# Optimization experiments

Measured on AMD Instinct MI355X. Metric: run time of the kernel, lower is better.

Reference implementation:

```python
import jax, jax.numpy as jnp
import numpy as np

B, LQ, S, D, H = 8, 1024, 256, 1024, 16
HD = D // H
LN_EPS = 1e-5


def layer_norm(x, g, b):
    m = jnp.mean(x, axis=-1, keepdims=True)
    v = jnp.mean((x - m) ** 2, axis=-1, keepdims=True)
    return (x - m) / jnp.sqrt(v + LN_EPS) * g + b


def setup_inputs() -> dict:
    key = jax.random.key(0)
    ks = jax.random.split(key, 12)
    sc = 0.02
    p = lambda k, shp: jax.random.normal(k, shp, dtype=jnp.float32) * sc
    return {
        "memory": jax.random.normal(ks[0], (B, LQ, D // 2), dtype=jnp.float32),
        "gaze_features": jax.random.normal(ks[1], (B, LQ, D // 2), dtype=jnp.float32),
        "text_features": jax.random.normal(ks[2], (B, S, D), dtype=jnp.float32),
        "w_in": p(ks[3], (3 * D, D)),  # packed q,k,v in_proj (torch MHA layout)
        "b_in": jnp.zeros((3 * D,), jnp.float32),
        "w_o": p(ks[4], (D, D)),
        "b_o": jnp.zeros((D,), jnp.float32),
        "w1": p(ks[5], (D, D)),
        "b1": jnp.zeros((D,), jnp.float32),
        "w2": p(ks[6], (D, D)),
        "b2": jnp.zeros((D,), jnp.float32),
        "g1": jnp.ones((D,), jnp.float32),
        "be1": jnp.zeros((D,), jnp.float32),
        "g2": jnp.ones((D,), jnp.float32),
        "be2": jnp.zeros((D,), jnp.float32),
    }


def reference(memory, gaze_features, text_features, w_in, b_in, w_o, b_o,
              w1, b1, w2, b2, g1, be1, g2, be2):
    combined = jnp.concatenate([memory, gaze_features], axis=-1)  # [B, LQ, D]
    wq, wk, wv = w_in[:D], w_in[D:2 * D], w_in[2 * D:]
    bq, bk, bv = b_in[:D], b_in[D:2 * D], b_in[2 * D:]

    q = (combined @ wq.T + bq).reshape(B, LQ, H, HD)
    k = (text_features @ wk.T + bk).reshape(B, S, H, HD)
    v = (text_features @ wv.T + bv).reshape(B, S, H, HD)

    scores = jnp.einsum("bqhd,bkhd->bhqk", q, k) / jnp.sqrt(jnp.float32(HD))
    attn_w = jax.nn.softmax(scores, axis=-1)
    ctx = jnp.einsum("bhqk,bkhd->bqhd", attn_w, v).reshape(B, LQ, D)
    attn_output = ctx @ w_o.T + b_o  # [B, LQ, D]

    # dual FFN branches share linear1/linear2 (as in the source); dropout = eval identity
    ffn = jax.nn.relu(attn_output @ w1.T + b1) @ w2.T + b2
    refpoint_embed = layer_norm(ffn, g1, be1)
    tgt = layer_norm(ffn, g2, be2)

    # vectorized box decode (replaces the per-element Python loop)
    s = jax.nn.sigmoid(attn_output[..., :4])
    xc, yc, w, h = s[..., 0], s[..., 1], s[..., 2], s[..., 3]
    init_box_proposal = jnp.stack(
        [xc - w / 2, yc - h / 2, xc + w / 2, yc + h / 2], axis=-1)  # [B, LQ, 4]

    return refpoint_embed, tgt, init_box_proposal
```

## Files before the change

### kernel.cpp

```cpp
#include <hip/hip_runtime.h>


typedef unsigned short u16;
typedef unsigned int u32;
typedef __bf16 bf16x8 __attribute__((ext_vector_type(8)));
typedef float f32x4 __attribute__((ext_vector_type(4)));
typedef u16 u16x4 __attribute__((ext_vector_type(4)));

struct CvtArgs { const void* in[15]; };

__device__ __forceinline__ u16 f2bf(float f) {
  u32 u = __builtin_bit_cast(u32, f);
  u += 0x7fffu + ((u >> 16) & 1u);
  return (u16)(u >> 16);
}
__device__ __forceinline__ float bf2f(u16 h) {
  u32 u = ((u32)h) << 16;
  return __builtin_bit_cast(float, u);
}

struct WsPtrs {
  u16 *c_mem, *c_gaze, *c_text, *c_win, *c_bin, *c_wo, *c_bo, *c_w1, *c_b1,
      *c_w2, *c_b2, *c_g1, *c_be1, *c_g2, *c_be2;
  u16 *q, *k, *v, *ctx, *woT, *wf, *bfb, *h1, *ffnb;
};
__device__ __forceinline__ WsPtrs wsp(u16* C) {
  WsPtrs w;
  w.c_mem = C;                 w.c_gaze = C + 4194304;   w.c_text = C + 8388608;
  w.c_win = C + 10485760;      w.c_bin = C + 13631488;   w.c_wo = C + 13634560;
  w.c_bo = C + 14683136;       w.c_w1 = C + 14684160;    w.c_b1 = C + 15732736;
  w.c_w2 = C + 15733760;       w.c_b2 = C + 16782336;    w.c_g1 = C + 16783360;
  w.c_be1 = C + 16784384;      w.c_g2 = C + 16785408;    w.c_be2 = C + 16786432;
  u16* B2 = C + 16787488;
  w.q = B2;                    w.k = B2 + 8388608;       w.v = B2 + 10485760;
  w.ctx = B2 + 12582912;
  w.woT = B2 + 20971520;
  w.wf  = B2 + 22020096;
  w.bfb = B2 + 23068672;
  w.h1  = B2 + 29360128;
  w.ffnb = B2;
  return w;
}

__device__ __forceinline__ void cvt_chunk(bool f32in, u16* dst,
                                          const void* const* srcs, u32 c8) {
  const u32 cum[16] = {0u, 4194304u, 8388608u, 10485760u, 13631488u, 13634560u,
                       14683136u, 14684160u, 15732736u, 15733760u, 16782336u,
                       16783360u, 16784384u, 16785408u, 16786432u, 16787456u};
  u32 base = c8 * 8u;
  int idx = 0;
#pragma unroll
  for (int i = 1; i < 15; ++i) if (base >= cum[i]) idx = i;
  u32 off = base - cum[idx];
  if (f32in) {
    const float* s = (const float*)srcs[idx] + off;
    float4 a = ((const float4*)s)[0];
    float4 b = ((const float4*)s)[1];
    u16 t[8] = {f2bf(a.x), f2bf(a.y), f2bf(a.z), f2bf(a.w),
                f2bf(b.x), f2bf(b.y), f2bf(b.z), f2bf(b.w)};
    *(uint4*)(dst + base) = *(const uint4*)t;
  } else {
    *(uint4*)(dst + base) = *(const uint4*)((const u16*)srcs[idx] + off);
  }
}

__global__ __launch_bounds__(256) void cvt_tr(CvtArgs a, u16* ws) {
  __shared__ u16 tile[128 * 136];
  const bool f32in = (((const u32*)a.in[11])[0] == 0x3F800000u);
  const int bid = blockIdx.x, tid = threadIdx.x;
  if (bid < 64) {
    WsPtrs w = wsp(ws);
    int tr = bid >> 3, tc = bid & 7;
#pragma unroll
    for (int p = 0; p < 8; ++p) {
      int t = p * 16 + (tid >> 4);
      int j8 = (tid & 15) * 8;
      u16 tmp[8];
      if (f32in) {
        const float* s = (const float*)a.in[5] + (size_t)(tr * 128 + t) * 1024 + tc * 128 + j8;
        float4 x = ((const float4*)s)[0], y = ((const float4*)s)[1];
        tmp[0]=f2bf(x.x); tmp[1]=f2bf(x.y); tmp[2]=f2bf(x.z); tmp[3]=f2bf(x.w);
        tmp[4]=f2bf(y.x); tmp[5]=f2bf(y.y); tmp[6]=f2bf(y.z); tmp[7]=f2bf(y.w);
      } else {
        *(uint4*)tmp = *(const uint4*)((const u16*)a.in[5] + (size_t)(tr * 128 + t) * 1024 + tc * 128 + j8);
      }
      *(uint4*)&tile[t * 136 + j8] = *(const uint4*)tmp;
    }
    __syncthreads();
#pragma unroll
    for (int p = 0; p < 8; ++p) {
      int j = p * 16 + (tid >> 4);
      int t8 = (tid & 15) * 8;
      u16 tmp[8];
#pragma unroll
      for (int i = 0; i < 8; ++i) tmp[i] = tile[(t8 + i) * 136 + j];
      *(uint4*)(w.woT + (size_t)(tc * 128 + j) * 1024 + tr * 128 + t8) = *(const uint4*)tmp;
    }
  } else {
    u32 c8 = (u32)(bid - 64) * 256u + tid;
    if (c8 < 2098432u) cvt_chunk(f32in, ws, a.in, c8);
  }
}

__device__ __forceinline__ void gemm_core(
    u16* sA, u16* sB,
    const u16* A0, const u16* A1, int Ksplit, int lda0, int lda1,
    const u16* W, const u16* bias, void* out, int N, int K,
    int mode, int lg, int m0, int n0)
{
  const int tid = threadIdx.x;
  const int wave = tid >> 6, lane = tid & 63;
  const int quad = lane >> 4, l16 = lane & 15;
  const int wm = wave >> 1, wn = wave & 1;

  f32x4 acc[4][4];
#pragma unroll
  for (int i = 0; i < 4; ++i)
#pragma unroll
    for (int j = 0; j < 4; ++j) acc[i][j] = (f32x4){0.f, 0.f, 0.f, 0.f};

  for (int k0 = 0; k0 < K; k0 += 128) {
#pragma unroll
    for (int qi = 0; qi < 8; ++qi) {
      int p = (wave * 8 + qi) * 64 + lane;
      int row = p >> 4;
      int c = (p & 15) ^ (row & 7);
      int gk = k0 + (c << 3);
      const u16* srcA = (gk < Ksplit) ? (A0 + (size_t)(m0 + row) * lda0 + gk)
                                      : (A1 + (size_t)(m0 + row) * lda1 + (gk - Ksplit));
      __builtin_amdgcn_global_load_lds(
          (const __attribute__((address_space(1))) void*)srcA,
          (__attribute__((address_space(3))) void*)&sA[(size_t)(wave * 8 + qi) * 512],
          16, 0, 0);
      const u16* srcB = W + (size_t)(n0 + row) * K + gk;
      __builtin_amdgcn_global_load_lds(
          (const __attribute__((address_space(1))) void*)srcB,
          (__attribute__((address_space(3))) void*)&sB[(size_t)(wave * 8 + qi) * 512],
          16, 0, 0);
    }
    __syncthreads();
#pragma unroll
    for (int ks = 0; ks < 4; ++ks) {
      const int ch = (ks << 2) + quad;
      bf16x8 af[4], bw[4];
#pragma unroll
      for (int i = 0; i < 4; ++i) {
        int row = wm * 64 + i * 16 + l16;
        af[i] = *(const bf16x8*)&sA[(row << 7) + ((ch ^ (row & 7)) << 3)];
      }
#pragma unroll
      for (int j = 0; j < 4; ++j) {
        int row = wn * 64 + j * 16 + l16;
        bw[j] = *(const bf16x8*)&sB[(row << 7) + ((ch ^ (row & 7)) << 3)];
      }
#pragma unroll
      for (int i = 0; i < 4; ++i)
#pragma unroll
        for (int j = 0; j < 4; ++j)
          acc[i][j] = __builtin_amdgcn_mfma_f32_16x16x32_bf16(af[i], bw[j], acc[i][j], 0, 0, 0);
    }
    __syncthreads();
  }

#pragma unroll
  for (int i = 0; i < 4; ++i) {
#pragma unroll
    for (int j = 0; j < 4; ++j) {
      int n = n0 + wn * 64 + j * 16 + l16;
      float bv = bias ? bf2f(bias[n]) : 0.f;
#pragma unroll
      for (int rr = 0; rr < 4; ++rr) {
        int m = m0 + wm * 64 + i * 16 + quad * 4 + rr;
        float val = acc[i][j][rr] + bv;
        if (mode == 1) val = fmaxf(val, 0.f);
        if (mode <= 1) {
          ((u16*)out)[(size_t)m * N + n] = f2bf(val);
        } else if (mode == 3) {
          int b = m >> lg, l = m & ((1 << lg) - 1);
          int h = n >> 6, d = n & 63;
          ((u16*)out)[((size_t)((b * 16 + h)) << (lg + 6)) + (l << 6) + d] = f2bf(val);
        } else {
          int b = m >> lg, s = m & ((1 << lg) - 1);
          int h = n >> 6, d = n & 63;
          ((u16*)out)[((size_t)(((b * 16 + h) << 6) + d) << lg) + s] = f2bf(val);
        }
      }
    }
  }
}

__global__ __launch_bounds__(256) void qkvwf(u16* ws) {
  __shared__ u16 lds[32768];
  WsPtrs w = wsp(ws);
  const int bid = blockIdx.x, tid = threadIdx.x;
  if (bid < 512) {
    gemm_core(lds, lds + 16384, w.c_mem, w.c_gaze, 512, 512, 512,
              w.c_win, w.c_bin, w.q, 1024, 1024, 3, 10,
              (bid >> 3) * 128, (bid & 7) * 128);
  } else if (bid < 640) {
    int u = bid - 512;
    gemm_core(lds, lds + 16384, w.c_text, w.c_text, 1024, 1024, 1024,
              w.c_win + 1048576, w.c_bin + 1024, w.k, 1024, 1024, 3, 8,
              (u >> 3) * 128, (u & 7) * 128);
  } else if (bid < 768) {
    int u = bid - 640;
    gemm_core(lds, lds + 16384, w.c_text, w.c_text, 1024, 1024, 1024,
              w.c_win + 2097152, w.c_bin + 2048, w.v, 1024, 1024, 4, 8,
              (u >> 3) * 128, (u & 7) * 128);
  } else if (bid < 832) {
    int u = bid - 768;
    gemm_core(lds, lds + 16384, w.c_w1, w.c_w1, 1024, 1024, 1024,
              w.woT, nullptr, w.wf, 1024, 1024, 0, 0,
              (u >> 3) * 128, (u & 7) * 128);
  } else {
    int i = (bid - 832) * 256 + tid;
    const u16* w1row = w.c_w1 + (size_t)i * 1024;
    float acc = bf2f(w.c_b1[i]);
    for (int kk = 0; kk < 1024; kk += 8) {
      bf16x8 wv = *(const bf16x8*)(w1row + kk);
      bf16x8 bv = *(const bf16x8*)(w.c_bo + kk);
#pragma unroll
      for (int j = 0; j < 8; ++j) acc += (float)wv[j] * (float)bv[j];
    }
    w.bfb[i] = f2bf(acc);
  }
}

__global__ __launch_bounds__(256) void attn_kernel(u16* ws) {
  __shared__ u16 sV[64 * 256];
  __shared__ u16 sKP[256 * 64];
  WsPtrs w = wsp(ws);
  const int tid = threadIdx.x;
  const int wave = tid >> 6, lane = tid & 63;
  const int quad = lane >> 4, l16 = lane & 15;
  const int qb = blockIdx.x & 15, bh = blockIdx.x >> 4;

  {
    int rr = tid >> 3, c8 = (tid & 7) << 3;
    const u16* kb = w.k + (size_t)bh * 16384;
#pragma unroll
    for (int p = 0; p < 8; ++p) {
      int row = p * 32 + rr;
      uint4 val = *(const uint4*)(kb + row * 64 + c8);
      *(uint4*)&sKP[(row << 6) + ((((c8 >> 3) ^ (row & 7))) << 3)] = val;
    }
    int r2 = tid >> 5, c8b = (tid & 31) << 3;
    const u16* vb = w.v + (size_t)bh * 16384;
#pragma unroll
    for (int p = 0; p < 8; ++p) {
      int row = p * 8 + r2;
      uint4 val = *(const uint4*)(vb + (row << 8) + c8b);
      *(uint4*)&sV[(row << 8) + ((((c8b >> 3) ^ (row & 7))) << 3)] = val;
    }
  }
  bf16x8 aq[2];
  {
    const u16* qrow = w.q + ((size_t)bh * 1024 + qb * 64 + wave * 16 + l16) * 64 + quad * 8;
    aq[0] = *(const bf16x8*)(qrow);
    aq[1] = *(const bf16x8*)(qrow + 32);
  }
  __syncthreads();

  f32x4 sc[16];
#pragma unroll
  for (int nt = 0; nt < 16; ++nt) sc[nt] = (f32x4){0.f, 0.f, 0.f, 0.f};
#pragma unroll
  for (int ks = 0; ks < 2; ++ks) {
    const int ch = (ks << 2) + quad;
#pragma unroll
    for (int nt = 0; nt < 16; ++nt) {
      int row = nt * 16 + l16;
      bf16x8 bk = *(const bf16x8*)&sKP[(row << 6) + ((ch ^ (row & 7)) << 3)];
      sc[nt] = __builtin_amdgcn_mfma_f32_16x16x32_bf16(aq[ks], bk, sc[nt], 0, 0, 0);
    }
  }
#pragma unroll
  for (int rr = 0; rr < 4; ++rr) {
    float mx = -1e30f;
#pragma unroll
    for (int nt = 0; nt < 16; ++nt) mx = fmaxf(mx, sc[nt][rr]);
    for (int off = 1; off < 16; off <<= 1) mx = fmaxf(mx, __shfl_xor(mx, off, 64));
    float sum = 0.f;
#pragma unroll
    for (int nt = 0; nt < 16; ++nt) {
      float p = __expf((sc[nt][rr] - mx) * 0.125f);
      sc[nt][rr] = p; sum += p;
    }
    for (int off = 1; off < 16; off <<= 1) sum += __shfl_xor(sum, off, 64);
    float inv = 1.f / sum;
#pragma unroll
    for (int nt = 0; nt < 16; ++nt) sc[nt][rr] *= inv;
  }
  __syncthreads();
#pragma unroll
  for (int nt = 0; nt < 16; ++nt)
#pragma unroll
    for (int rr = 0; rr < 4; ++rr) {
      int row = wave * 16 + quad * 4 + rr;
      int col = nt * 16 + l16;
      sKP[(row << 8) + (((col >> 3) ^ (row & 7)) << 3) + (col & 7)] = f2bf(sc[nt][rr]);
    }
  __syncthreads();

  f32x4 o[4];
#pragma unroll
  for (int j = 0; j < 4; ++j) o[j] = (f32x4){0.f, 0.f, 0.f, 0.f};
#pragma unroll
  for (int ks = 0; ks < 8; ++ks) {
    const int ch = (ks << 2) + quad;
    int prow = wave * 16 + l16;
    bf16x8 ap = *(const bf16x8*)&sKP[(prow << 8) + ((ch ^ (prow & 7)) << 3)];
#pragma unroll
    for (int j = 0; j < 4; ++j) {
      int vrow = j * 16 + l16;
      bf16x8 bv = *(const bf16x8*)&sV[(vrow << 8) + ((ch ^ (vrow & 7)) << 3)];
      o[j] = __builtin_amdgcn_mfma_f32_16x16x32_bf16(ap, bv, o[j], 0, 0, 0);
    }
  }
  const int b = bh >> 4, h = bh & 15;
#pragma unroll
  for (int j = 0; j < 4; ++j)
#pragma unroll
    for (int rr = 0; rr < 4; ++rr) {
      int m = qb * 64 + wave * 16 + quad * 4 + rr;
      int d = h * 64 + j * 16 + l16;
      w.ctx[((size_t)b * 1024 + m) * 1024 + d] = f2bf(o[j][rr]);
    }
}

__global__ __launch_bounds__(256) void h1box(u16* ws, void* out, const void* g1orig) {
  __shared__ u16 lds[32768];
  WsPtrs w = wsp(ws);
  const int u = blockIdx.x, tid = threadIdx.x;
  const int r16 = tid >> 4, l4 = tid & 15;
  {
    const bool f32out = (((const u32*)g1orig)[0] == 0x3F800000u);
    int m = u * 16 + r16;
    int k0 = l4 * 64;
    const u16* crow = w.ctx + (size_t)m * 1024 + k0;
    float a0 = 0.f, a1 = 0.f, a2 = 0.f, a3 = 0.f;
#pragma unroll
    for (int kk = 0; kk < 64; kk += 8) {
      bf16x8 cv = *(const bf16x8*)(crow + kk);
      bf16x8 w0 = *(const bf16x8*)(w.c_wo + k0 + kk);
      bf16x8 w1 = *(const bf16x8*)(w.c_wo + 1024 + k0 + kk);
      bf16x8 w2 = *(const bf16x8*)(w.c_wo + 2048 + k0 + kk);
      bf16x8 w3 = *(const bf16x8*)(w.c_wo + 3072 + k0 + kk);
#pragma unroll
      for (int j = 0; j < 8; ++j) {
        float c = (float)cv[j];
        a0 += c * (float)w0[j]; a1 += c * (float)w1[j];
        a2 += c * (float)w2[j]; a3 += c * (float)w3[j];
      }
    }
    for (int off = 1; off < 16; off <<= 1) {
      a0 += __shfl_xor(a0, off, 64); a1 += __shfl_xor(a1, off, 64);
      a2 += __shfl_xor(a2, off, 64); a3 += __shfl_xor(a3, off, 64);
    }
    if (l4 == 0) {
      a0 += bf2f(w.c_bo[0]); a1 += bf2f(w.c_bo[1]);
      a2 += bf2f(w.c_bo[2]); a3 += bf2f(w.c_bo[3]);
      float s0 = 1.f / (1.f + __expf(-a0)), s1 = 1.f / (1.f + __expf(-a1));
      float s2 = 1.f / (1.f + __expf(-a2)), s3 = 1.f / (1.f + __expf(-a3));
      float o0 = s0 - s2 * 0.5f, o1 = s1 - s3 * 0.5f;
      float o2 = s0 + s2 * 0.5f, o3 = s1 + s3 * 0.5f;
      if (f32out) {
        float* fo = (float*)out + 16777216;
        *(float4*)(fo + (size_t)m * 4) = make_float4(o0, o1, o2, o3);
      } else {
        u16* bo = (u16*)out + 16777216;
        u16x4 o; o[0] = f2bf(o0); o[1] = f2bf(o1); o[2] = f2bf(o2); o[3] = f2bf(o3);
        *(u16x4*)(bo + (size_t)m * 4) = o;
      }
    }
  }
  gemm_core(lds, lds + 16384, w.ctx, w.ctx, 1024, 1024, 1024,
            w.wf, w.bfb, w.h1, 1024, 1024, 1, 0, (u >> 3) * 128, (u & 7) * 128);
}

__global__ __launch_bounds__(256) void w2gemm(u16* ws) {
  __shared__ u16 lds[32768];
  WsPtrs w = wsp(ws);
  gemm_core(lds, lds + 16384, w.h1, w.h1, 1024, 1024, 1024,
            w.c_w2, w.c_b2, w.ffnb, 1024, 1024, 0, 0,
            (blockIdx.x >> 3) * 128, (blockIdx.x & 7) * 128);
}

__global__ __launch_bounds__(256) void ln_kernel(u16* ws, void* outv, const void* g1orig) {
  WsPtrs w = wsp(ws);
  const bool f32out = (((const u32*)g1orig)[0] == 0x3F800000u);
  const int row = blockIdx.x, tid = threadIdx.x;
  int c = tid * 4;
  u16x4 xr = *(const u16x4*)(w.ffnb + (size_t)row * 1024 + c);
  float x[4] = {bf2f(xr[0]), bf2f(xr[1]), bf2f(xr[2]), bf2f(xr[3])};
  float s = x[0] + x[1] + x[2] + x[3];
  float s2 = x[0]*x[0] + x[1]*x[1] + x[2]*x[2] + x[3]*x[3];
  for (int m = 32; m >= 1; m >>= 1) { s += __shfl_xor(s, m, 64); s2 += __shfl_xor(s2, m, 64); }
  __shared__ float red[8];
  int wv = tid >> 6;
  if ((tid & 63) == 0) { red[wv] = s; red[4 + wv] = s2; }
  __syncthreads();
  s = red[0] + red[1] + red[2] + red[3];
  s2 = red[4] + red[5] + red[6] + red[7];
  float mean = s * (1.f / 1024.f);
  float var = s2 * (1.f / 1024.f) - mean * mean;
  float inv = rsqrtf(var + 1e-5f);
  float y[4] = {(x[0] - mean) * inv, (x[1] - mean) * inv, (x[2] - mean) * inv, (x[3] - mean) * inv};
  float v1[4], v2[4];
#pragma unroll
  for (int i = 0; i < 4; ++i) {
    v1[i] = y[i] * bf2f(w.c_g1[c + i]) + bf2f(w.c_be1[c + i]);
    v2[i] = y[i] * bf2f(w.c_g2[c + i]) + bf2f(w.c_be2[c + i]);
  }
  if (f32out) {
    float* fo = (float*)outv;
    *(float4*)(fo + (size_t)row * 1024 + c) = make_float4(v1[0], v1[1], v1[2], v1[3]);
    *(float4*)(fo + 8388608 + (size_t)row * 1024 + c) = make_float4(v2[0], v2[1], v2[2], v2[3]);
  } else {
    u16* out = (u16*)outv;
    u16x4 o1, o2;
#pragma unroll
    for (int i = 0; i < 4; ++i) { o1[i] = f2bf(v1[i]); o2[i] = f2bf(v2[i]); }
    *(u16x4*)(out + (size_t)row * 1024 + c) = o1;
    *(u16x4*)(out + 8388608 + (size_t)row * 1024 + c) = o2;
  }
}

extern "C" void kernel_launch(void* const* d_in, const int* in_sizes, int n_in,
                              void* d_out, int out_size, void* d_ws, size_t ws_size,
                              hipStream_t stream) {
  CvtArgs ca;
  for (int i = 0; i < 15; ++i) ca.in[i] = d_in[i];
  u16* ws = (u16*)d_ws;
  dim3 blk(256);
  cvt_tr<<<dim3(8261), blk, 0, stream>>>(ca, ws);
  qkvwf<<<dim3(836), blk, 0, stream>>>(ws);
  attn_kernel<<<dim3(2048), blk, 0, stream>>>(ws);
  h1box<<<dim3(512), blk, 0, stream>>>(ws, d_out, d_in[11]);
  w2gemm<<<dim3(512), blk, 0, stream>>>(ws);
  ln_kernel<<<dim3(8192), blk, 0, stream>>>(ws, d_out, d_in[11]);
}
```

Measured before the change: 296.9 us.

## Replace 128x128 GEMM core with double-buffered 256x256 tile, 8-wave pipelined kernel

Replaces the single-buffered 128x128 GEMM with a 256x256 output tile computed by 8 waves. It double-buffers 64-wide K slices in 128KB of LDS, prefetching the next slice while MFMAs run, with explicit vmcnt waits, barriers and setprio. The goal is more operand reuse per byte loaded and overlap of global loads with compute. The cost is far fewer blocks: 128 per M=8192 GEMM, and only 32 each for the K and V projections, which can leave CUs idle on a 256-CU part. Block-to-tile mappings and the box-decode row split are adjusted to match.

```diff
diff --git a/kernel.cpp b/kernel.cpp
--- a/kernel.cpp
+++ b/kernel.cpp
@@ -102,118 +102,152 @@
   }
 }
 
-__device__ __forceinline__ void gemm_core(
-    u16* sA, u16* sB,
+__device__ __forceinline__ void stage_half(
+    u16* dst, const u16* P0, const u16* P1, int Ksplit, int ld0, int ld1,
+    int rowbase, int k0, int tid) {
+#pragma unroll
+  for (int r = 0; r < 2; ++r) {
+    int p = (r << 9) + tid;
+    int rr = p >> 3;
+    int gk = k0 + ((((p & 7) ^ (rr & 7))) << 3);
+    const u16* src = (gk < Ksplit)
+        ? P0 + (size_t)(rowbase + rr) * ld0 + gk
+        : P1 + (size_t)(rowbase + rr) * ld1 + (gk - Ksplit);
+    __builtin_amdgcn_global_load_lds(
+        (const __attribute__((address_space(1))) void*)src,
+        (__attribute__((address_space(3))) void*)(dst + ((size_t)p << 3)),
+        16, 0, 0);
+  }
+}
+
+__device__ __forceinline__ void gemm256(
+    u16* lds,
     const u16* A0, const u16* A1, int Ksplit, int lda0, int lda1,
-    const u16* W, const u16* bias, void* out, int N, int K,
-    int mode, int lg, int m0, int n0)
-{
+    const u16* W, const u16* bias, u16* out, int N, int K,
+    int mode, int lg, int m0, int n0) {
   const int tid = threadIdx.x;
-  const int wave = tid >> 6, lane = tid & 63;
+  const int lane = tid & 63;
   const int quad = lane >> 4, l16 = lane & 15;
-  const int wm = wave >> 1, wn = wave & 1;
-
-  f32x4 acc[4][4];
-#pragma unroll
-  for (int i = 0; i < 4; ++i)
-#pragma unroll
-    for (int j = 0; j < 4; ++j) acc[i][j] = (f32x4){0.f, 0.f, 0.f, 0.f};
-
-  for (int k0 = 0; k0 < K; k0 += 128) {
-#pragma unroll
-    for (int qi = 0; qi < 8; ++qi) {
-      int p = (wave * 8 + qi) * 64 + lane;
-      int row = p >> 4;
-      int c = (p & 15) ^ (row & 7);
-      int gk = k0 + (c << 3);
-      const u16* srcA = (gk < Ksplit) ? (A0 + (size_t)(m0 + row) * lda0 + gk)
-                                      : (A1 + (size_t)(m0 + row) * lda1 + (gk - Ksplit));
-      __builtin_amdgcn_global_load_lds(
-          (const __attribute__((address_space(1))) void*)srcA,
-          (__attribute__((address_space(3))) void*)&sA[(size_t)(wave * 8 + qi) * 512],
-          16, 0, 0);
-      const u16* srcB = W + (size_t)(n0 + row) * K + gk;
-      __builtin_amdgcn_global_load_lds(
-          (const __attribute__((address_space(1))) void*)srcB,
-          (__attribute__((address_space(3))) void*)&sB[(size_t)(wave * 8 + qi) * 512],
-          16, 0, 0);
-    }
-    __syncthreads();
-#pragma unroll
-    for (int ks = 0; ks < 4; ++ks) {
-      const int ch = (ks << 2) + quad;
-      bf16x8 af[4], bw[4];
+  const int wave = tid >> 6;
+  const int wm = wave >> 2, wn = wave & 3;
+  const int BIGK = 0x40000000;
+  const int NT = K >> 6;
+
+  u16* sA0b = lds;
+  u16* sB0b = lds + 32768;
+
+  f32x4 acc[2][4][2][2];
+#pragma unroll
+  for (int h = 0; h < 2; ++h)
+#pragma unroll
+    for (int i = 0; i < 4; ++i)
+#pragma unroll
+      for (int g = 0; g < 2; ++g)
+#pragma unroll
+        for (int j = 0; j < 2; ++j)
+          acc[h][i][g][j] = (f32x4){0.f, 0.f, 0.f, 0.f};
+
+  stage_half(sA0b,        A0, A1, Ksplit, lda0, lda1, m0,       0, tid);
+  stage_half(sB0b,        W,  W,  BIGK,   K,    K,    n0,       0, tid);
+  stage_half(sB0b + 8192, W,  W,  BIGK,   K,    K,    n0 + 128, 0, tid);
+  stage_half(sA0b + 8192, A0, A1, Ksplit, lda0, lda1, m0 + 128, 0, tid);
+  asm volatile("s_waitcnt vmcnt(4)" ::: "memory");
+  __builtin_amdgcn_s_barrier();
+  __builtin_amdgcn_sched_barrier(0);
+
+  for (int T = 0; T < NT; ++T) {
+    u16* sAc = lds + ((T & 1) << 14);
+    u16* sBc = lds + 32768 + ((T & 1) << 14);
+    u16* sAn = lds + (((T + 1) & 1) << 14);
+    u16* sBn = lds + 32768 + (((T + 1) & 1) << 14);
+    const bool more = (T + 1 < NT);
+    const int k0n = (T + 1) << 6;
+#pragma unroll
+    for (int p = 0; p < 4; ++p) {
+      const int h = p >> 1, g = p & 1;
+      bf16x8 af[4][2], bw[2][2];
 #pragma unroll
       for (int i = 0; i < 4; ++i) {
-        int row = wm * 64 + i * 16 + l16;
-        af[i] = *(const bf16x8*)&sA[(row << 7) + ((ch ^ (row & 7)) << 3)];
-      }
-#pragma unroll
-      for (int j = 0; j < 4; ++j) {
-        int row = wn * 64 + j * 16 + l16;
-        bw[j] = *(const bf16x8*)&sB[(row << 7) + ((ch ^ (row & 7)) << 3)];
-      }
+        const int rr = wm * 64 + i * 16 + l16;
+        const int sw = rr & 7;
+#pragma unroll
+        for (int ks = 0; ks < 2; ++ks)
+          af[i][ks] = *(const bf16x8*)(sAc + (h << 13) + (rr << 6) + (((ks * 4 + quad) ^ sw) << 3));
+      }
+#pragma unroll
+      for (int j = 0; j < 2; ++j) {
+        const int rr = wn * 32 + j * 16 + l16;
+        const int sw = rr & 7;
+#pragma unroll
+        for (int ks = 0; ks < 2; ++ks)
+          bw[j][ks] = *(const bf16x8*)(sBc + (g << 13) + (rr << 6) + (((ks * 4 + quad) ^ sw) << 3));
+      }
+      if (more && p == 0) {
+        stage_half(sAn, A0, A1, Ksplit, lda0, lda1, m0, k0n, tid);
+        stage_half(sBn, W, W, BIGK, K, K, n0, k0n, tid);
+      }
+      if (more && p == 1) {
+        stage_half(sBn + 8192, W, W, BIGK, K, K, n0 + 128, k0n, tid);
+        stage_half(sAn + 8192, A0, A1, Ksplit, lda0, lda1, m0 + 128, k0n, tid);
+      }
+      __builtin_amdgcn_s_barrier();
+      __builtin_amdgcn_sched_barrier(0);
+      __builtin_amdgcn_s_setprio(1);
 #pragma unroll
       for (int i = 0; i < 4; ++i)
 #pragma unroll
-        for (int j = 0; j < 4; ++j)
-          acc[i][j] = __builtin_amdgcn_mfma_f32_16x16x32_bf16(af[i], bw[j], acc[i][j], 0, 0, 0);
-    }
-    __syncthreads();
-  }
-
-#pragma unroll
-  for (int i = 0; i < 4; ++i) {
-#pragma unroll
-    for (int j = 0; j < 4; ++j) {
-      int n = n0 + wn * 64 + j * 16 + l16;
-      float bv = bias ? bf2f(bias[n]) : 0.f;
-#pragma unroll
-      for (int rr = 0; rr < 4; ++rr) {
-        int m = m0 + wm * 64 + i * 16 + quad * 4 + rr;
-        float val = acc[i][j][rr] + bv;
-        if (mode == 1) val = fmaxf(val, 0.f);
-        if (mode <= 1) {
-          ((u16*)out)[(size_t)m * N + n] = f2bf(val);
-        } else if (mode == 3) {
-          int b = m >> lg, l = m & ((1 << lg) - 1);
-          int h = n >> 6, d = n & 63;
-          ((u16*)out)[((size_t)((b * 16 + h)) << (lg + 6)) + (l << 6) + d] = f2bf(val);
-        } else {
-          int b = m >> lg, s = m & ((1 << lg) - 1);
-          int h = n >> 6, d = n & 63;
-          ((u16*)out)[((size_t)(((b * 16 + h) << 6) + d) << lg) + s] = f2bf(val);
+        for (int j = 0; j < 2; ++j)
+#pragma unroll
+          for (int ks = 0; ks < 2; ++ks)
+            acc[h][i][g][j] = __builtin_amdgcn_mfma_f32_16x16x32_bf16(
+                af[i][ks], bw[j][ks], acc[h][i][g][j], 0, 0, 0);
+      __builtin_amdgcn_s_setprio(0);
+      if (p == 0) {
+        if (more) asm volatile("s_waitcnt vmcnt(4)" ::: "memory");
+        else      asm volatile("s_waitcnt vmcnt(0)" ::: "memory");
+      }
+      if (p == 3 && more) asm volatile("s_waitcnt vmcnt(4)" ::: "memory");
+      __builtin_amdgcn_s_barrier();
+      __builtin_amdgcn_sched_barrier(0);
+    }
+  }
+
+#pragma unroll
+  for (int h = 0; h < 2; ++h)
+#pragma unroll
+    for (int i = 0; i < 4; ++i)
+#pragma unroll
+      for (int g = 0; g < 2; ++g)
+#pragma unroll
+        for (int j = 0; j < 2; ++j) {
+          const int n = n0 + g * 128 + wn * 32 + j * 16 + l16;
+          const float bv = bias ? bf2f(bias[n]) : 0.f;
+#pragma unroll
+          for (int rr4 = 0; rr4 < 4; ++rr4) {
+            const int m = m0 + h * 128 + wm * 64 + i * 16 + quad * 4 + rr4;
+            float val = acc[h][i][g][j][rr4] + bv;
+            if (mode == 1) val = fmaxf(val, 0.f);
+            if (mode <= 1) {
+              out[(size_t)m * N + n] = f2bf(val);
+            } else if (mode == 3) {
+              int b = m >> lg, l = m & ((1 << lg) - 1);
+              int hh = n >> 6, d = n & 63;
+              out[((size_t)(b * 16 + hh) << (lg + 6)) + ((size_t)l << 6) + d] = f2bf(val);
+            } else {
+              int b = m >> lg, s = m & ((1 << lg) - 1);
+              int hh = n >> 6, d = n & 63;
+              out[((size_t)(((b * 16 + hh) << 6) + d) << lg) + s] = f2bf(val);
+            }
+          }
         }
-      }
-    }
-  }
-}
-
-__global__ __launch_bounds__(256) void qkvwf(u16* ws) {
-  __shared__ u16 lds[32768];
+}
+
+__global__ __launch_bounds__(512, 2) void qkvwf(u16* ws) {
+  __shared__ __align__(16) u16 lds[65536];
   WsPtrs w = wsp(ws);
   const int bid = blockIdx.x, tid = threadIdx.x;
-  if (bid < 512) {
-    gemm_core(lds, lds + 16384, w.c_mem, w.c_gaze, 512, 512, 512,
-              w.c_win, w.c_bin, w.q, 1024, 1024, 3, 10,
-              (bid >> 3) * 128, (bid & 7) * 128);
-  } else if (bid < 640) {
-    int u = bid - 512;
-    gemm_core(lds, lds + 16384, w.c_text, w.c_text, 1024, 1024, 1024,
-              w.c_win + 1048576, w.c_bin + 1024, w.k, 1024, 1024, 3, 8,
-              (u >> 3) * 128, (u & 7) * 128);
-  } else if (bid < 768) {
-    int u = bid - 640;
-    gemm_core(lds, lds + 16384, w.c_text, w.c_text, 1024, 1024, 1024,
-              w.c_win + 2097152, w.c_bin + 2048, w.v, 1024, 1024, 4, 8,
-              (u >> 3) * 128, (u & 7) * 128);
-  } else if (bid < 832) {
-    int u = bid - 768;
-    gemm_core(lds, lds + 16384, w.c_w1, w.c_w1, 1024, 1024, 1024,
-              w.woT, nullptr, w.wf, 1024, 1024, 0, 0,
-              (u >> 3) * 128, (u & 7) * 128);
-  } else {
-    int i = (bid - 832) * 256 + tid;
+  if (bid >= 208) {
+    int i = (bid - 208) * 512 + tid;
     const u16* w1row = w.c_w1 + (size_t)i * 1024;
     float acc = bf2f(w.c_b1[i]);
     for (int kk = 0; kk < 1024; kk += 8) {
@@ -223,7 +257,32 @@
       for (int j = 0; j < 8; ++j) acc += (float)wv[j] * (float)bv[j];
     }
     w.bfb[i] = f2bf(acc);
-  }
+    return;
+  }
+  const u16 *A0, *A1, *W, *bias; u16* out;
+  int Ksplit, lda0, lda1, mode, lg, m0, n0;
+  if (bid < 128) {
+    A0 = w.c_mem; A1 = w.c_gaze; Ksplit = 512; lda0 = 512; lda1 = 512;
+    W = w.c_win; bias = w.c_bin; out = w.q; mode = 3; lg = 10;
+    m0 = (bid >> 2) * 256; n0 = (bid & 3) * 256;
+  } else if (bid < 160) {
+    int u = bid - 128;
+    A0 = w.c_text; A1 = w.c_text; Ksplit = 1024; lda0 = 1024; lda1 = 1024;
+    W = w.c_win + 1048576; bias = w.c_bin + 1024; out = w.k; mode = 3; lg = 8;
+    m0 = (u >> 2) * 256; n0 = (u & 3) * 256;
+  } else if (bid < 192) {
+    int u = bid - 160;
+    A0 = w.c_text; A1 = w.c_text; Ksplit = 1024; lda0 = 1024; lda1 = 1024;
+    W = w.c_win + 2097152; bias = w.c_bin + 2048; out = w.v; mode = 4; lg = 8;
+    m0 = (u >> 2) * 256; n0 = (u & 3) * 256;
+  } else {
+    int u = bid - 192;
+    A0 = w.c_w1; A1 = w.c_w1; Ksplit = 1024; lda0 = 1024; lda1 = 1024;
+    W = w.woT; bias = nullptr; out = w.wf; mode = 0; lg = 0;
+    m0 = (u >> 2) * 256; n0 = (u & 3) * 256;
+  }
+  gemm256(lds, A0, A1, Ksplit, lda0, lda1, W, bias, out, 1024, 1024,
+          mode, lg, m0, n0);
 }
 
 __global__ __launch_bounds__(256) void attn_kernel(u16* ws) {
@@ -328,36 +387,36 @@
     }
 }
 
-__global__ __launch_bounds__(256) void h1box(u16* ws, void* out, const void* g1orig) {
-  __shared__ u16 lds[32768];
+__global__ __launch_bounds__(512, 2) void h1box(u16* ws, void* out, const void* g1orig) {
+  __shared__ __align__(16) u16 lds[65536];
   WsPtrs w = wsp(ws);
   const int u = blockIdx.x, tid = threadIdx.x;
-  const int r16 = tid >> 4, l4 = tid & 15;
   {
     const bool f32out = (((const u32*)g1orig)[0] == 0x3F800000u);
-    int m = u * 16 + r16;
-    int k0 = l4 * 64;
+    int m = u * 64 + (tid >> 3);
+    int l8 = tid & 7;
+    int k0 = l8 * 128;
     const u16* crow = w.ctx + (size_t)m * 1024 + k0;
     float a0 = 0.f, a1 = 0.f, a2 = 0.f, a3 = 0.f;
 #pragma unroll
-    for (int kk = 0; kk < 64; kk += 8) {
+    for (int kk = 0; kk < 128; kk += 8) {
       bf16x8 cv = *(const bf16x8*)(crow + kk);
       bf16x8 w0 = *(const bf16x8*)(w.c_wo + k0 + kk);
-      bf16x8 w1 = *(const bf16x8*)(w.c_wo + 1024 + k0 + kk);
-      bf16x8 w2 = *(const bf16x8*)(w.c_wo + 2048 + k0 + kk);
-      bf16x8 w3 = *(const bf16x8*)(w.c_wo + 3072 + k0 + kk);
+      bf16x8 w1v = *(const bf16x8*)(w.c_wo + 1024 + k0 + kk);
+      bf16x8 w2v = *(const bf16x8*)(w.c_wo + 2048 + k0 + kk);
+      bf16x8 w3v = *(const bf16x8*)(w.c_wo + 3072 + k0 + kk);
 #pragma unroll
       for (int j = 0; j < 8; ++j) {
         float c = (float)cv[j];
-        a0 += c * (float)w0[j]; a1 += c * (float)w1[j];
-        a2 += c * (float)w2[j]; a3 += c * (float)w3[j];
-      }
-    }
-    for (int off = 1; off < 16; off <<= 1) {
+        a0 += c * (float)w0[j]; a1 += c * (float)w1v[j];
+        a2 += c * (float)w2v[j]; a3 += c * (float)w3v[j];
+      }
+    }
+    for (int off = 1; off < 8; off <<= 1) {
       a0 += __shfl_xor(a0, off, 64); a1 += __shfl_xor(a1, off, 64);
       a2 += __shfl_xor(a2, off, 64); a3 += __shfl_xor(a3, off, 64);
     }
-    if (l4 == 0) {
+    if (l8 == 0) {
       a0 += bf2f(w.c_bo[0]); a1 += bf2f(w.c_bo[1]);
       a2 += bf2f(w.c_bo[2]); a3 += bf2f(w.c_bo[3]);
       float s0 = 1.f / (1.f + __expf(-a0)), s1 = 1.f / (1.f + __expf(-a1));
@@ -374,16 +433,15 @@
       }
     }
   }
-  gemm_core(lds, lds + 16384, w.ctx, w.ctx, 1024, 1024, 1024,
-            w.wf, w.bfb, w.h1, 1024, 1024, 1, 0, (u >> 3) * 128, (u & 7) * 128);
-}
-
-__global__ __launch_bounds__(256) void w2gemm(u16* ws) {
-  __shared__ u16 lds[32768];
+  gemm256(lds, w.ctx, w.ctx, 0x40000000, 1024, 1024, w.wf, w.bfb, w.h1,
+          1024, 1024, 1, 0, (u >> 2) * 256, (u & 3) * 256);
+}
+
+__global__ __launch_bounds__(512, 2) void w2gemm(u16* ws) {
+  __shared__ __align__(16) u16 lds[65536];
   WsPtrs w = wsp(ws);
-  gemm_core(lds, lds + 16384, w.h1, w.h1, 1024, 1024, 1024,
-            w.c_w2, w.c_b2, w.ffnb, 1024, 1024, 0, 0,
-            (blockIdx.x >> 3) * 128, (blockIdx.x & 7) * 128);
+  gemm256(lds, w.h1, w.h1, 0x40000000, 1024, 1024, w.c_w2, w.c_b2, w.ffnb,
+          1024, 1024, 0, 0, (blockIdx.x >> 2) * 256, (blockIdx.x & 3) * 256);
 }
 
 __global__ __launch_bounds__(256) void ln_kernel(u16* ws, void* outv, const void* g1orig) {
@@ -432,11 +490,10 @@
   CvtArgs ca;
   for (int i = 0; i < 15; ++i) ca.in[i] = d_in[i];
   u16* ws = (u16*)d_ws;
-  dim3 blk(256);
-  cvt_tr<<<dim3(8261), blk, 0, stream>>>(ca, ws);
-  qkvwf<<<dim3(836), blk, 0, stream>>>(ws);
-  attn_kernel<<<dim3(2048), blk, 0, stream>>>(ws);
-  h1box<<<dim3(512), blk, 0, stream>>>(ws, d_out, d_in[11]);
-  w2gemm<<<dim3(512), blk, 0, stream>>>(ws);
-  ln_kernel<<<dim3(8192), blk, 0, stream>>>(ws, d_out, d_in[11]);
-}
+  cvt_tr<<<dim3(8261), dim3(256), 0, stream>>>(ca, ws);
+  qkvwf<<<dim3(210), dim3(512), 0, stream>>>(ws);
+  attn_kernel<<<dim3(2048), dim3(256), 0, stream>>>(ws);
+  h1box<<<dim3(128), dim3(512), 0, stream>>>(ws, d_out, d_in[11]);
+  w2gemm<<<dim3(128), dim3(512), 0, stream>>>(ws);
+  ln_kernel<<<dim3(8192), dim3(256), 0, stream>>>(ws, d_out, d_in[11]);
+}
```

Result: slower. 340.1 us (+14.5%).
